# Kernel optimization log

Hardware: AMD Instinct MI355X
Metric: run time of the kernel (lower is better)

Reference implementation:

```python
import jax, jax.numpy as jnp
import numpy as np

B, N_NODES, N_MEM, DEG, D, R = 64, 50000, 65536, 4, 128, 500
E = N_MEM * DEG


def _mlp2(x, W1, b1, W2, b2):
    # F layer with n_layers=2: Dense(leaky_relu) -> Dense(tanh); tf.nn.leaky_relu alpha=0.2
    h = jax.nn.leaky_relu(x @ W1 + b1, negative_slope=0.2)
    return jnp.tanh(h @ W2 + b2)


def setup_inputs() -> dict:
    key = jax.random.key(0)
    ks = jax.random.split(key, 17)
    eg_e = jax.random.randint(ks[0], (E,), 0, B)
    rel = jax.random.randint(ks[1], (E,), 0, R)
    e2vi = jax.random.randint(ks[2], (E,), 0, N_MEM)
    idx_vi = jax.random.randint(ks[3], (E,), 0, N_MEM)
    # every memorized node receives DEG edges; new_idx_e2vj == idx_vj (DPMPN invariant)
    idx_vj = jnp.tile(jnp.arange(N_MEM), DEG)
    z = jnp.zeros((E,), jnp.int32)
    seen_edges = jnp.stack([eg_e, z, z, rel, idx_vi, idx_vj, e2vi, idx_vj], axis=1).astype(jnp.int32)
    eg_m = jax.random.randint(ks[4], (N_MEM,), 0, B)
    v_m = jax.random.randint(ks[5], (N_MEM,), 0, N_NODES)
    memorized_nodes = jnp.stack([eg_m, v_m], axis=1).astype(jnp.int32)
    s = 0.05
    return {
        'hidden': jax.random.normal(ks[6], (N_MEM, D), jnp.float32),
        'seen_edges': seen_edges,
        'memorized_nodes': memorized_nodes,
        'node_attention': jax.random.uniform(ks[7], (B, N_NODES), jnp.float32),
        'hidden_uncon': jax.random.normal(ks[8], (1, N_NODES, D), jnp.float32),
        'query_head_emb': jax.random.normal(ks[9], (B, D), jnp.float32),
        'query_rel_emb': jax.random.normal(ks[10], (B, D), jnp.float32),
        'rel_table': jax.random.normal(ks[11], (R, D), jnp.float32),
        'msg_W1': jax.random.normal(ks[12], (5 * D, D), jnp.float32) * s,
        'msg_b1': jnp.zeros((D,), jnp.float32),
        'msg_W2': jax.random.normal(ks[13], (D, D), jnp.float32) * s,
        'msg_b2': jnp.zeros((D,), jnp.float32),
        'hid_W1': jax.random.normal(ks[14], (5 * D, D), jnp.float32) * s,
        'hid_b1': jnp.zeros((D,), jnp.float32),
        'hid_W2': jax.random.normal(ks[15], (D, D), jnp.float32) * s,
        'hid_b2': jnp.zeros((D,), jnp.float32),
        'int_W': jax.random.normal(ks[16], (D, D), jnp.float32) * s,
    }


def reference(hidden, seen_edges, memorized_nodes, node_attention, hidden_uncon,
              query_head_emb, query_rel_emb, rel_table,
              msg_W1, msg_b1, msg_W2, msg_b2,
              hid_W1, hid_b1, hid_W2, hid_b2, int_W):
    n_mem = hidden.shape[0]
    # node2edge: gather endpoint features to edges
    eg_e = seen_edges[:, 0]
    hidden_vi = hidden[seen_edges[:, 6]]
    hidden_vj = hidden[seen_edges[:, 7]]
    rel_emb = rel_table[seen_edges[:, 3]]
    qh_e = query_head_emb[eg_e]
    qr_e = query_rel_emb[eg_e]
    msg_in = jnp.concatenate([hidden_vi, rel_emb, hidden_vj, qh_e, qr_e], axis=-1)  # [E, 5D]
    message = _mlp2(msg_in, msg_W1, msg_b1, msg_W2, msg_b2)  # [E, D]
    # aggregate at vj, aggr_op 'mean_v3': unsorted_segment_mean * sqrt(count), then scatter
    idx_vj = seen_edges[:, 5]
    seg_sum = jax.ops.segment_sum(message, idx_vj, num_segments=n_mem)
    cnt = jax.ops.segment_sum(jnp.ones((E,), message.dtype), idx_vj, num_segments=n_mem)
    aggr = seg_sum * (jnp.sqrt(cnt) / jnp.maximum(cnt, 1.0))[:, None]
    red = jax.ops.segment_max(seen_edges[:, 7], idx_vj, num_segments=n_mem)
    nonempty = cnt > 0
    red = jnp.where(nonempty, red, 0)
    message_aggr = jnp.zeros_like(hidden).at[red].add(jnp.where(nonempty[:, None], aggr, 0.0))
    # unconscious-flow intervention per memorized node
    eg_m = memorized_nodes[:, 0]
    v_m = memorized_nodes[:, 1]
    hu = hidden_uncon[0][v_m]  # [n_mem, D]
    na = node_attention[eg_m, v_m]  # [n_mem]
    hu = (na[:, None] * hu) @ int_W
    qh_m = query_head_emb[eg_m]
    qr_m = query_rel_emb[eg_m]
    upd_in = jnp.concatenate([message_aggr, hidden, hu, qh_m, qr_m], axis=-1)  # [n_mem, 5D]
    update = _mlp2(upd_in, hid_W1, hid_b1, hid_W2, hid_b2)
    return hidden + update
```

## Files before the change

kernel.cpp:

```cpp
#include <hip/hip_runtime.h>
#include <hip/hip_bf16.h>

typedef unsigned short u16;
typedef __attribute__((ext_vector_type(8))) short bf16x8;
typedef __attribute__((ext_vector_type(4))) float f32x4;

#define N_MEM_C 65536
#define NNODES_C 50000
#define DDIM 128
#define LDA 136
#define BM 128
#define TIL(t) ((t) * 16384)

__device__ __align__(16) u16 g_WT[7 * 16384];
__device__ __align__(16) float g_relW[500 * 128];
__device__ __align__(16) float g_qsumM[64 * 128];
__device__ __align__(16) float g_qsumH[64 * 128];

__device__ __forceinline__ u16 f2bf_s(float f) {
  __hip_bfloat16 h = __float2bfloat16(f);
  u16 u; __builtin_memcpy(&u, &h, 2);
  return u;
}
__device__ __forceinline__ unsigned pk2(float a, float b) {
  __hip_bfloat162 h = __float22bfloat162_rn(make_float2(a, b));
  unsigned u; __builtin_memcpy(&u, &h, 4);
  return u;
}
__device__ __forceinline__ float fast_tanh(float x) {
  float e = __expf(2.0f * x);
  return 1.0f - 2.0f / (e + 1.0f);
}

extern "C" __global__ void prep_wt(const float* __restrict__ msg_W1,
                                   const float* __restrict__ msg_W2,
                                   const float* __restrict__ hid_W1,
                                   const float* __restrict__ hid_W2) {
  int i = blockIdx.x * 256 + threadIdx.x;
  int t = i >> 14, idx = i & 16383;
  int n = idx >> 7, k = idx & 127;
  const float* src; int dst;
  switch (t) {
    case 0:  src = msg_W1;             dst = TIL(0); break;
    case 1:  src = msg_W1 + 256 * 128; dst = TIL(1); break;
    case 2:  src = msg_W2;             dst = TIL(2); break;
    case 3:  src = hid_W1;             dst = TIL(3); break;
    case 4:  src = hid_W1 + 128 * 128; dst = TIL(4); break;
    default: src = hid_W2;             dst = TIL(6); break;
  }
  g_WT[dst + n * 128 + k] = f2bf_s(src[k * 128 + n]);
}

extern "C" __global__ void prep_weff(const float* __restrict__ hid_W1,
                                     const float* __restrict__ int_W) {
  int i = blockIdx.x * 256 + threadIdx.x;
  int n = i & 127, q = i >> 7;
  float s = 0.f;
  for (int p = 0; p < 128; ++p)
    s += int_W[q * 128 + p] * hid_W1[(256 + p) * 128 + n];
  g_WT[TIL(5) + n * 128 + q] = f2bf_s(s);
}

extern "C" __global__ void prep_relW(const float* __restrict__ rel_table,
                                     const float* __restrict__ msg_W1) {
  int i = blockIdx.x * 256 + threadIdx.x;
  if (i >= 500 * 128) return;
  int r = i >> 7, n = i & 127;
  float s = 0.f;
  for (int k = 0; k < 128; ++k)
    s += rel_table[r * 128 + k] * msg_W1[(128 + k) * 128 + n];
  g_relW[i] = s;
}

extern "C" __global__ void prep_qsum(const float* __restrict__ qh,
                                     const float* __restrict__ qr,
                                     const float* __restrict__ msg_W1,
                                     const float* __restrict__ hid_W1) {
  int i = blockIdx.x * 256 + threadIdx.x;
  int g = i >> 7, n = i & 127;
  float sM = 0.f, sH = 0.f;
  for (int k = 0; k < 128; ++k) {
    float h = qh[g * 128 + k], r = qr[g * 128 + k];
    sM += h * msg_W1[(384 + k) * 128 + n] + r * msg_W1[(512 + k) * 128 + n];
    sH += h * hid_W1[(384 + k) * 128 + n] + r * hid_W1[(512 + k) * 128 + n];
  }
  g_qsumM[i] = sM;
  g_qsumH[i] = sH;
}

template <int MODE>
__device__ __forceinline__ void stage_rows(u16 (*A)[LDA], const float* __restrict__ src,
                                           const int* idxArr, const float* scArr,
                                           int base, int tid) {
#pragma unroll
  for (int it = 0; it < 4; ++it) {
    int slot = it * 256 + tid;
    int r = slot >> 3, seg = slot & 7;
    int idx = (MODE == 1) ? (base + r) : idxArr[r];
    float sc = (MODE == 2) ? scArr[r] : 1.0f;
    const float4* p = (const float4*)(src + (size_t)idx * DDIM + seg * 16);
    float4 f0 = p[0], f1 = p[1], f2 = p[2], f3 = p[3];
    if (MODE == 2) {
      f0.x *= sc; f0.y *= sc; f0.z *= sc; f0.w *= sc;
      f1.x *= sc; f1.y *= sc; f1.z *= sc; f1.w *= sc;
      f2.x *= sc; f2.y *= sc; f2.z *= sc; f2.w *= sc;
      f3.x *= sc; f3.y *= sc; f3.z *= sc; f3.w *= sc;
    }
    uint4* q = (uint4*)&A[r][seg * 16];
    q[0] = make_uint4(pk2(f0.x, f0.y), pk2(f0.z, f0.w), pk2(f1.x, f1.y), pk2(f1.z, f1.w));
    q[1] = make_uint4(pk2(f2.x, f2.y), pk2(f2.z, f2.w), pk2(f3.x, f3.y), pk2(f3.z, f3.w));
  }
}

__device__ __forceinline__ void stage_w(u16 (*W)[LDA], const u16* __restrict__ WT, int tid) {
#pragma unroll
  for (int it = 0; it < 2; ++it) {
    int slot = it * 256 + tid;
    int n = slot >> 2, seg = slot & 3;
    const uint4* p = (const uint4*)(WT + n * 128 + seg * 32);
    uint4 a = p[0], b = p[1], c = p[2], d = p[3];
    uint4* q = (uint4*)&W[n][seg * 32];
    q[0] = a; q[1] = b; q[2] = c; q[3] = d;
  }
}

__device__ __forceinline__ void gemm128(const u16 (*A)[LDA], const u16 (*W)[LDA],
                                        f32x4 (&acc)[4][4], int wr, int wc, int l16, int l4) {
#pragma unroll
  for (int ks = 0; ks < 4; ++ks) {
    bf16x8 av[4], bv[4];
#pragma unroll
    for (int mr = 0; mr < 4; ++mr)
      av[mr] = *(const bf16x8*)&A[wr * 64 + mr * 16 + l16][ks * 32 + l4 * 8];
#pragma unroll
    for (int nr = 0; nr < 4; ++nr)
      bv[nr] = *(const bf16x8*)&W[wc * 64 + nr * 16 + l16][ks * 32 + l4 * 8];
#pragma unroll
    for (int mr = 0; mr < 4; ++mr)
#pragma unroll
      for (int nr = 0; nr < 4; ++nr)
        acc[mr][nr] = __builtin_amdgcn_mfma_f32_16x16x32_bf16(av[mr], bv[nr], acc[mr][nr], 0, 0, 0);
  }
}

extern "C" __global__ __launch_bounds__(256, 2) void fused_flow(
    const float* __restrict__ hidden, const int* __restrict__ seen_edges,
    const int* __restrict__ memorized, const float* __restrict__ node_att,
    const float* __restrict__ hidden_uncon,
    const float* __restrict__ msg_b1, const float* __restrict__ msg_b2,
    const float* __restrict__ hid_b1, const float* __restrict__ hid_b2,
    float* __restrict__ out) {
  __shared__ u16 sA[BM][LDA];
  __shared__ u16 sW[DDIM][LDA];
  __shared__ int sI0[BM];
  __shared__ int sI1[BM];
  __shared__ int sI2[BM];
  __shared__ float sNA[BM];

  const int tid = threadIdx.x;
  const int lane = tid & 63, wid = tid >> 6;
  const int wr = wid >> 1, wc = wid & 1;
  const int l16 = lane & 15, l4 = lane >> 4;
  const int j0 = blockIdx.x * BM;

  float mb1v[4], mb2v[4], hb1v[4], hb2v[4];
#pragma unroll
  for (int nr = 0; nr < 4; ++nr) {
    int col = wc * 64 + nr * 16 + l16;
    mb1v[nr] = msg_b1[col]; mb2v[nr] = msg_b2[col];
    hb1v[nr] = hid_b1[col]; hb2v[nr] = hid_b2[col];
  }

  const f32x4 zero4 = {0.f, 0.f, 0.f, 0.f};

  stage_rows<1>(sA, hidden, nullptr, nullptr, j0, tid);
  stage_w(sW, g_WT + TIL(1), tid);
  __syncthreads();
  f32x4 acc_vj[4][4];
#pragma unroll
  for (int a = 0; a < 4; ++a)
#pragma unroll
    for (int b = 0; b < 4; ++b) acc_vj[a][b] = zero4;
  gemm128(sA, sW, acc_vj, wr, wc, l16, l4);

  f32x4 aggr[4][4];
#pragma unroll
  for (int a = 0; a < 4; ++a)
#pragma unroll
    for (int b = 0; b < 4; ++b) aggr[a][b] = zero4;

#pragma unroll 1
  for (int t = 0; t < 4; ++t) {
    __syncthreads();
    if (tid < BM) {
      int e = j0 + tid + t * N_MEM_C;
      const int4* se = (const int4*)seen_edges + (size_t)e * 2;
      int4 lo = se[0], hi = se[1];
      int eg = min(max(lo.x, 0), 63);
      int rl = min(max(lo.w, 0), 499);
      int vi = min(max(hi.z, 0), N_MEM_C - 1);
      sI0[tid] = eg; sI1[tid] = rl; sI2[tid] = vi;
    }
    __syncthreads();

    stage_rows<0>(sA, hidden, sI2, nullptr, 0, tid);
    stage_w(sW, g_WT + TIL(0), tid);
    __syncthreads();
    f32x4 acc[4][4];
#pragma unroll
    for (int a = 0; a < 4; ++a)
#pragma unroll
      for (int b = 0; b < 4; ++b) acc[a][b] = acc_vj[a][b];
    gemm128(sA, sW, acc, wr, wc, l16, l4);

#pragma unroll
    for (int mr = 0; mr < 4; ++mr)
#pragma unroll
      for (int i = 0; i < 4; ++i) {
        int r = wr * 64 + mr * 16 + l4 * 4 + i;
        const float* pr = g_relW + sI1[r] * 128;
        const float* pq = g_qsumM + sI0[r] * 128;
#pragma unroll
        for (int nr = 0; nr < 4; ++nr) {
          int c = wc * 64 + nr * 16 + l16;
          acc[mr][nr][i] += pr[c] + pq[c];
        }
      }
    __syncthreads();

#pragma unroll
    for (int mr = 0; mr < 4; ++mr)
#pragma unroll
      for (int nr = 0; nr < 4; ++nr)
#pragma unroll
        for (int i = 0; i < 4; ++i) {
          float v = acc[mr][nr][i] + mb1v[nr];
          v = (v >= 0.f) ? v : 0.2f * v;
          sA[wr * 64 + mr * 16 + l4 * 4 + i][wc * 64 + nr * 16 + l16] = f2bf_s(v);
        }
    stage_w(sW, g_WT + TIL(2), tid);
    __syncthreads();

    f32x4 acc2[4][4];
#pragma unroll
    for (int a = 0; a < 4; ++a)
#pragma unroll
      for (int b = 0; b < 4; ++b) acc2[a][b] = zero4;
    gemm128(sA, sW, acc2, wr, wc, l16, l4);
#pragma unroll
    for (int mr = 0; mr < 4; ++mr)
#pragma unroll
      for (int nr = 0; nr < 4; ++nr)
#pragma unroll
        for (int i = 0; i < 4; ++i)
          aggr[mr][nr][i] += fast_tanh(acc2[mr][nr][i] + mb2v[nr]);
  }

  __syncthreads();
  if (tid < BM) {
    int2 mn = ((const int2*)memorized)[j0 + tid];
    int eg = min(max(mn.x, 0), 63);
    int vm = min(max(mn.y, 0), NNODES_C - 1);
    sI0[tid] = eg; sI2[tid] = vm;
    sNA[tid] = node_att[(size_t)eg * NNODES_C + vm];
  }
#pragma unroll
  for (int mr = 0; mr < 4; ++mr)
#pragma unroll
    for (int nr = 0; nr < 4; ++nr)
#pragma unroll
      for (int i = 0; i < 4; ++i)
        sA[wr * 64 + mr * 16 + l4 * 4 + i][wc * 64 + nr * 16 + l16] =
            f2bf_s(0.5f * aggr[mr][nr][i]);
  stage_w(sW, g_WT + TIL(3), tid);
  __syncthreads();
  f32x4 accU[4][4];
#pragma unroll
  for (int a = 0; a < 4; ++a)
#pragma unroll
    for (int b = 0; b < 4; ++b) accU[a][b] = zero4;
  gemm128(sA, sW, accU, wr, wc, l16, l4);
  __syncthreads();

  stage_rows<1>(sA, hidden, nullptr, nullptr, j0, tid);
  stage_w(sW, g_WT + TIL(4), tid);
  __syncthreads();
  gemm128(sA, sW, accU, wr, wc, l16, l4);
  __syncthreads();

  stage_rows<2>(sA, hidden_uncon, sI2, sNA, 0, tid);
  stage_w(sW, g_WT + TIL(5), tid);
  __syncthreads();
  gemm128(sA, sW, accU, wr, wc, l16, l4);

#pragma unroll
  for (int mr = 0; mr < 4; ++mr)
#pragma unroll
    for (int i = 0; i < 4; ++i) {
      int r = wr * 64 + mr * 16 + l4 * 4 + i;
      const float* pq = g_qsumH + sI0[r] * 128;
#pragma unroll
      for (int nr = 0; nr < 4; ++nr)
        accU[mr][nr][i] += pq[wc * 64 + nr * 16 + l16];
    }
  __syncthreads();

#pragma unroll
  for (int mr = 0; mr < 4; ++mr)
#pragma unroll
    for (int nr = 0; nr < 4; ++nr)
#pragma unroll
      for (int i = 0; i < 4; ++i) {
        float v = accU[mr][nr][i] + hb1v[nr];
        v = (v >= 0.f) ? v : 0.2f * v;
        sA[wr * 64 + mr * 16 + l4 * 4 + i][wc * 64 + nr * 16 + l16] = f2bf_s(v);
      }
  stage_w(sW, g_WT + TIL(6), tid);
  __syncthreads();

  f32x4 acc2[4][4];
#pragma unroll
  for (int a = 0; a < 4; ++a)
#pragma unroll
    for (int b = 0; b < 4; ++b) acc2[a][b] = zero4;
  gemm128(sA, sW, acc2, wr, wc, l16, l4);

#pragma unroll
  for (int mr = 0; mr < 4; ++mr)
#pragma unroll
    for (int nr = 0; nr < 4; ++nr)
#pragma unroll
      for (int i = 0; i < 4; ++i) {
        int row = j0 + wr * 64 + mr * 16 + l4 * 4 + i;
        int col = wc * 64 + nr * 16 + l16;
        size_t o = (size_t)row * DDIM + col;
        out[o] = hidden[o] + fast_tanh(acc2[mr][nr][i] + hb2v[nr]);
      }
}

extern "C" void kernel_launch(void* const* d_in, const int* in_sizes, int n_in,
                              void* d_out, int out_size, void* d_ws, size_t ws_size,
                              hipStream_t stream) {
  (void)in_sizes; (void)n_in; (void)out_size; (void)d_ws; (void)ws_size;
  const float* hidden       = (const float*)d_in[0];
  const int*   seen_edges   = (const int*)d_in[1];
  const int*   memorized    = (const int*)d_in[2];
  const float* node_att     = (const float*)d_in[3];
  const float* hidden_uncon = (const float*)d_in[4];
  const float* qh           = (const float*)d_in[5];
  const float* qr           = (const float*)d_in[6];
  const float* rel_table    = (const float*)d_in[7];
  const float* msg_W1       = (const float*)d_in[8];
  const float* msg_b1       = (const float*)d_in[9];
  const float* msg_W2       = (const float*)d_in[10];
  const float* msg_b2       = (const float*)d_in[11];
  const float* hid_W1       = (const float*)d_in[12];
  const float* hid_b1       = (const float*)d_in[13];
  const float* hid_W2       = (const float*)d_in[14];
  const float* hid_b2       = (const float*)d_in[15];
  const float* int_W        = (const float*)d_in[16];

  prep_wt<<<dim3(6 * 16384 / 256), dim3(256), 0, stream>>>(msg_W1, msg_W2, hid_W1, hid_W2);
  prep_weff<<<dim3(64), dim3(256), 0, stream>>>(hid_W1, int_W);
  prep_relW<<<dim3(250), dim3(256), 0, stream>>>(rel_table, msg_W1);
  prep_qsum<<<dim3(32), dim3(256), 0, stream>>>(qh, qr, msg_W1, hid_W1);
  fused_flow<<<dim3(N_MEM_C / BM), dim3(256), 0, stream>>>(
      hidden, seen_edges, memorized, node_att, hidden_uncon,
      msg_b1, msg_b2, hid_b1, hid_b2, (float*)d_out);
}
```

Baseline: 146.5 us.

## Read weight B-fragments from global directly, drop LDS weight tile, use 512 threads

Removes the shared-memory weight tile and loads MFMA B operands straight from the pre-transposed global bf16 weights, relying on L2/L1 caching. The block grows to 512 threads (8 waves, 4 column groups of 32), with fewer accumulators per thread and lower LDS use, aimed at higher occupancy. All edge and memorized-node indices are loaded up front, removing per-iteration index loads and several barriers. The cost is uncoalesced per-lane global loads of weights on every GEMM step, with latency exposed inside the MFMA loop.

```diff
diff --git a/kernel.cpp b/kernel.cpp
--- a/kernel.cpp
+++ b/kernel.cpp
@@ -10,6 +10,7 @@
 #define DDIM 128
 #define LDA 136
 #define BM 128
+#define NTHR 512
 #define TIL(t) ((t) * 16384)
 
 __device__ __align__(16) u16 g_WT[7 * 16384];
@@ -93,8 +94,8 @@
                                            const int* idxArr, const float* scArr,
                                            int base, int tid) {
 #pragma unroll
-  for (int it = 0; it < 4; ++it) {
-    int slot = it * 256 + tid;
+  for (int it = 0; it < 2; ++it) {
+    int slot = it * NTHR + tid;
     int r = slot >> 3, seg = slot & 7;
     int idx = (MODE == 1) ? (base + r) : idxArr[r];
     float sc = (MODE == 2) ? scArr[r] : 1.0f;
@@ -112,38 +113,27 @@
   }
 }
 
-__device__ __forceinline__ void stage_w(u16 (*W)[LDA], const u16* __restrict__ WT, int tid) {
-#pragma unroll
-  for (int it = 0; it < 2; ++it) {
-    int slot = it * 256 + tid;
-    int n = slot >> 2, seg = slot & 3;
-    const uint4* p = (const uint4*)(WT + n * 128 + seg * 32);
-    uint4 a = p[0], b = p[1], c = p[2], d = p[3];
-    uint4* q = (uint4*)&W[n][seg * 32];
-    q[0] = a; q[1] = b; q[2] = c; q[3] = d;
-  }
-}
-
-__device__ __forceinline__ void gemm128(const u16 (*A)[LDA], const u16 (*W)[LDA],
-                                        f32x4 (&acc)[4][4], int wr, int wc, int l16, int l4) {
+__device__ __forceinline__ void gemm128g(const u16 (*A)[LDA], const u16* __restrict__ WT,
+                                         f32x4 (&acc)[4][2], int wr, int wc, int l16, int l4) {
+  const u16* wb = WT + (wc * 32 + l16) * 128 + l4 * 8;
 #pragma unroll
   for (int ks = 0; ks < 4; ++ks) {
-    bf16x8 av[4], bv[4];
+    bf16x8 av[4], bv[2];
+#pragma unroll
+    for (int nr = 0; nr < 2; ++nr)
+      bv[nr] = *(const bf16x8*)(wb + nr * 16 * 128 + ks * 32);
 #pragma unroll
     for (int mr = 0; mr < 4; ++mr)
       av[mr] = *(const bf16x8*)&A[wr * 64 + mr * 16 + l16][ks * 32 + l4 * 8];
 #pragma unroll
-    for (int nr = 0; nr < 4; ++nr)
-      bv[nr] = *(const bf16x8*)&W[wc * 64 + nr * 16 + l16][ks * 32 + l4 * 8];
-#pragma unroll
-    for (int mr = 0; mr < 4; ++mr)
-#pragma unroll
-      for (int nr = 0; nr < 4; ++nr)
+    for (int mr = 0; mr < 4; ++mr)
+#pragma unroll
+      for (int nr = 0; nr < 2; ++nr)
         acc[mr][nr] = __builtin_amdgcn_mfma_f32_16x16x32_bf16(av[mr], bv[nr], acc[mr][nr], 0, 0, 0);
   }
 }
 
-extern "C" __global__ __launch_bounds__(256, 2) void fused_flow(
+extern "C" __global__ __launch_bounds__(NTHR, 4) void fused_flow(
     const float* __restrict__ hidden, const int* __restrict__ seen_edges,
     const int* __restrict__ memorized, const float* __restrict__ node_att,
     const float* __restrict__ hidden_uncon,
@@ -151,78 +141,77 @@
     const float* __restrict__ hid_b1, const float* __restrict__ hid_b2,
     float* __restrict__ out) {
   __shared__ u16 sA[BM][LDA];
-  __shared__ u16 sW[DDIM][LDA];
-  __shared__ int sI0[BM];
-  __shared__ int sI1[BM];
-  __shared__ int sI2[BM];
+  __shared__ int sEg[4][BM];
+  __shared__ int sRel[4][BM];
+  __shared__ int sVi[4][BM];
+  __shared__ int sMeg[BM];
+  __shared__ int sMvm[BM];
   __shared__ float sNA[BM];
 
   const int tid = threadIdx.x;
   const int lane = tid & 63, wid = tid >> 6;
-  const int wr = wid >> 1, wc = wid & 1;
+  const int wr = wid >> 2, wc = wid & 3;
   const int l16 = lane & 15, l4 = lane >> 4;
   const int j0 = blockIdx.x * BM;
 
-  float mb1v[4], mb2v[4], hb1v[4], hb2v[4];
-#pragma unroll
-  for (int nr = 0; nr < 4; ++nr) {
-    int col = wc * 64 + nr * 16 + l16;
+  float mb1v[2], mb2v[2], hb1v[2], hb2v[2];
+#pragma unroll
+  for (int nr = 0; nr < 2; ++nr) {
+    int col = wc * 32 + nr * 16 + l16;
     mb1v[nr] = msg_b1[col]; mb2v[nr] = msg_b2[col];
     hb1v[nr] = hid_b1[col]; hb2v[nr] = hid_b2[col];
   }
 
+  {
+    int t = tid >> 7, r = tid & 127;
+    int e = j0 + r + t * N_MEM_C;
+    const int4* se = (const int4*)seen_edges + (size_t)e * 2;
+    int4 lo = se[0], hi = se[1];
+    sEg[t][r] = min(max(lo.x, 0), 63);
+    sRel[t][r] = min(max(lo.w, 0), 499);
+    sVi[t][r] = min(max(hi.z, 0), N_MEM_C - 1);
+  }
+  if (tid < BM) {
+    int2 mn = ((const int2*)memorized)[j0 + tid];
+    int eg = min(max(mn.x, 0), 63);
+    int vm = min(max(mn.y, 0), NNODES_C - 1);
+    sMeg[tid] = eg; sMvm[tid] = vm;
+    sNA[tid] = node_att[(size_t)eg * NNODES_C + vm];
+  }
+  stage_rows<1>(sA, hidden, nullptr, nullptr, j0, tid);
+  __syncthreads();
+
   const f32x4 zero4 = {0.f, 0.f, 0.f, 0.f};
-
-  stage_rows<1>(sA, hidden, nullptr, nullptr, j0, tid);
-  stage_w(sW, g_WT + TIL(1), tid);
-  __syncthreads();
-  f32x4 acc_vj[4][4];
+  f32x4 acc_vj[4][2], aggr[4][2];
 #pragma unroll
   for (int a = 0; a < 4; ++a)
 #pragma unroll
-    for (int b = 0; b < 4; ++b) acc_vj[a][b] = zero4;
-  gemm128(sA, sW, acc_vj, wr, wc, l16, l4);
-
-  f32x4 aggr[4][4];
-#pragma unroll
-  for (int a = 0; a < 4; ++a)
-#pragma unroll
-    for (int b = 0; b < 4; ++b) aggr[a][b] = zero4;
+    for (int b = 0; b < 2; ++b) { acc_vj[a][b] = zero4; aggr[a][b] = zero4; }
+  gemm128g(sA, g_WT + TIL(1), acc_vj, wr, wc, l16, l4);
 
 #pragma unroll 1
   for (int t = 0; t < 4; ++t) {
     __syncthreads();
-    if (tid < BM) {
-      int e = j0 + tid + t * N_MEM_C;
-      const int4* se = (const int4*)seen_edges + (size_t)e * 2;
-      int4 lo = se[0], hi = se[1];
-      int eg = min(max(lo.x, 0), 63);
-      int rl = min(max(lo.w, 0), 499);
-      int vi = min(max(hi.z, 0), N_MEM_C - 1);
-      sI0[tid] = eg; sI1[tid] = rl; sI2[tid] = vi;
-    }
+    stage_rows<0>(sA, hidden, sVi[t], nullptr, 0, tid);
     __syncthreads();
 
-    stage_rows<0>(sA, hidden, sI2, nullptr, 0, tid);
-    stage_w(sW, g_WT + TIL(0), tid);
-    __syncthreads();
-    f32x4 acc[4][4];
+    f32x4 acc[4][2];
 #pragma unroll
     for (int a = 0; a < 4; ++a)
 #pragma unroll
-      for (int b = 0; b < 4; ++b) acc[a][b] = acc_vj[a][b];
-    gemm128(sA, sW, acc, wr, wc, l16, l4);
+      for (int b = 0; b < 2; ++b) acc[a][b] = acc_vj[a][b];
+    gemm128g(sA, g_WT + TIL(0), acc, wr, wc, l16, l4);
 
 #pragma unroll
     for (int mr = 0; mr < 4; ++mr)
 #pragma unroll
       for (int i = 0; i < 4; ++i) {
         int r = wr * 64 + mr * 16 + l4 * 4 + i;
-        const float* pr = g_relW + sI1[r] * 128;
-        const float* pq = g_qsumM + sI0[r] * 128;
-#pragma unroll
-        for (int nr = 0; nr < 4; ++nr) {
-          int c = wc * 64 + nr * 16 + l16;
+        const float* pr = g_relW + sRel[t][r] * 128;
+        const float* pq = g_qsumM + sEg[t][r] * 128;
+#pragma unroll
+        for (int nr = 0; nr < 2; ++nr) {
+          int c = wc * 32 + nr * 16 + l16;
           acc[mr][nr][i] += pr[c] + pq[c];
         }
       }
@@ -231,108 +220,96 @@
 #pragma unroll
     for (int mr = 0; mr < 4; ++mr)
 #pragma unroll
-      for (int nr = 0; nr < 4; ++nr)
+      for (int nr = 0; nr < 2; ++nr)
 #pragma unroll
         for (int i = 0; i < 4; ++i) {
           float v = acc[mr][nr][i] + mb1v[nr];
           v = (v >= 0.f) ? v : 0.2f * v;
-          sA[wr * 64 + mr * 16 + l4 * 4 + i][wc * 64 + nr * 16 + l16] = f2bf_s(v);
+          sA[wr * 64 + mr * 16 + l4 * 4 + i][wc * 32 + nr * 16 + l16] = f2bf_s(v);
         }
-    stage_w(sW, g_WT + TIL(2), tid);
     __syncthreads();
 
-    f32x4 acc2[4][4];
+    f32x4 acc2[4][2];
 #pragma unroll
     for (int a = 0; a < 4; ++a)
 #pragma unroll
-      for (int b = 0; b < 4; ++b) acc2[a][b] = zero4;
-    gemm128(sA, sW, acc2, wr, wc, l16, l4);
-#pragma unroll
-    for (int mr = 0; mr < 4; ++mr)
-#pragma unroll
-      for (int nr = 0; nr < 4; ++nr)
+      for (int b = 0; b < 2; ++b) acc2[a][b] = zero4;
+    gemm128g(sA, g_WT + TIL(2), acc2, wr, wc, l16, l4);
+#pragma unroll
+    for (int mr = 0; mr < 4; ++mr)
+#pragma unroll
+      for (int nr = 0; nr < 2; ++nr)
 #pragma unroll
         for (int i = 0; i < 4; ++i)
           aggr[mr][nr][i] += fast_tanh(acc2[mr][nr][i] + mb2v[nr]);
   }
 
   __syncthreads();
-  if (tid < BM) {
-    int2 mn = ((const int2*)memorized)[j0 + tid];
-    int eg = min(max(mn.x, 0), 63);
-    int vm = min(max(mn.y, 0), NNODES_C - 1);
-    sI0[tid] = eg; sI2[tid] = vm;
-    sNA[tid] = node_att[(size_t)eg * NNODES_C + vm];
-  }
 #pragma unroll
   for (int mr = 0; mr < 4; ++mr)
 #pragma unroll
-    for (int nr = 0; nr < 4; ++nr)
+    for (int nr = 0; nr < 2; ++nr)
 #pragma unroll
       for (int i = 0; i < 4; ++i)
-        sA[wr * 64 + mr * 16 + l4 * 4 + i][wc * 64 + nr * 16 + l16] =
+        sA[wr * 64 + mr * 16 + l4 * 4 + i][wc * 32 + nr * 16 + l16] =
             f2bf_s(0.5f * aggr[mr][nr][i]);
-  stage_w(sW, g_WT + TIL(3), tid);
-  __syncthreads();
-  f32x4 accU[4][4];
+  __syncthreads();
+  f32x4 accU[4][2];
 #pragma unroll
   for (int a = 0; a < 4; ++a)
 #pragma unroll
-    for (int b = 0; b < 4; ++b) accU[a][b] = zero4;
-  gemm128(sA, sW, accU, wr, wc, l16, l4);
+    for (int b = 0; b < 2; ++b) accU[a][b] = zero4;
+  gemm128g(sA, g_WT + TIL(3), accU, wr, wc, l16, l4);
   __syncthreads();
 
   stage_rows<1>(sA, hidden, nullptr, nullptr, j0, tid);
-  stage_w(sW, g_WT + TIL(4), tid);
-  __syncthreads();
-  gemm128(sA, sW, accU, wr, wc, l16, l4);
-  __syncthreads();
-
-  stage_rows<2>(sA, hidden_uncon, sI2, sNA, 0, tid);
-  stage_w(sW, g_WT + TIL(5), tid);
-  __syncthreads();
-  gemm128(sA, sW, accU, wr, wc, l16, l4);
+  __syncthreads();
+  gemm128g(sA, g_WT + TIL(4), accU, wr, wc, l16, l4);
+  __syncthreads();
+
+  stage_rows<2>(sA, hidden_uncon, sMvm, sNA, 0, tid);
+  __syncthreads();
+  gemm128g(sA, g_WT + TIL(5), accU, wr, wc, l16, l4);
 
 #pragma unroll
   for (int mr = 0; mr < 4; ++mr)
 #pragma unroll
     for (int i = 0; i < 4; ++i) {
       int r = wr * 64 + mr * 16 + l4 * 4 + i;
-      const float* pq = g_qsumH + sI0[r] * 128;
-#pragma unroll
-      for (int nr = 0; nr < 4; ++nr)
-        accU[mr][nr][i] += pq[wc * 64 + nr * 16 + l16];
+      const float* pq = g_qsumH + sMeg[r] * 128;
+#pragma unroll
+      for (int nr = 0; nr < 2; ++nr)
+        accU[mr][nr][i] += pq[wc * 32 + nr * 16 + l16];
     }
   __syncthreads();
 
 #pragma unroll
   for (int mr = 0; mr < 4; ++mr)
 #pragma unroll
-    for (int nr = 0; nr < 4; ++nr)
+    for (int nr = 0; nr < 2; ++nr)
 #pragma unroll
       for (int i = 0; i < 4; ++i) {
         float v = accU[mr][nr][i] + hb1v[nr];
         v = (v >= 0.f) ? v : 0.2f * v;
-        sA[wr * 64 + mr * 16 + l4 * 4 + i][wc * 64 + nr * 16 + l16] = f2bf_s(v);
+        sA[wr * 64 + mr * 16 + l4 * 4 + i][wc * 32 + nr * 16 + l16] = f2bf_s(v);
       }
-  stage_w(sW, g_WT + TIL(6), tid);
-  __syncthreads();
-
-  f32x4 acc2[4][4];
+  __syncthreads();
+
+  f32x4 acc2[4][2];
 #pragma unroll
   for (int a = 0; a < 4; ++a)
 #pragma unroll
-    for (int b = 0; b < 4; ++b) acc2[a][b] = zero4;
-  gemm128(sA, sW, acc2, wr, wc, l16, l4);
+    for (int b = 0; b < 2; ++b) acc2[a][b] = zero4;
+  gemm128g(sA, g_WT + TIL(6), acc2, wr, wc, l16, l4);
 
 #pragma unroll
   for (int mr = 0; mr < 4; ++mr)
 #pragma unroll
-    for (int nr = 0; nr < 4; ++nr)
+    for (int nr = 0; nr < 2; ++nr)
 #pragma unroll
       for (int i = 0; i < 4; ++i) {
         int row = j0 + wr * 64 + mr * 16 + l4 * 4 + i;
-        int col = wc * 64 + nr * 16 + l16;
+        int col = wc * 32 + nr * 16 + l16;
         size_t o = (size_t)row * DDIM + col;
         out[o] = hidden[o] + fast_tanh(acc2[mr][nr][i] + hb2v[nr]);
       }
@@ -364,7 +341,7 @@
   prep_weff<<<dim3(64), dim3(256), 0, stream>>>(hid_W1, int_W);
   prep_relW<<<dim3(250), dim3(256), 0, stream>>>(rel_table, msg_W1);
   prep_qsum<<<dim3(32), dim3(256), 0, stream>>>(qh, qr, msg_W1, hid_W1);
-  fused_flow<<<dim3(N_MEM_C / BM), dim3(256), 0, stream>>>(
+  fused_flow<<<dim3(N_MEM_C / BM), dim3(NTHR), 0, stream>>>(
       hidden, seen_edges, memorized, node_att, hidden_uncon,
       msg_b1, msg_b2, hid_b1, hid_b2, (float*)d_out);
 }
```

Result: slower. 172.4 us (+17.7%).
